# Performance work log

Measured on AMD Instinct MI355X. Metric: run time of the kernel, lower is better.

The kernel has to match this reference:

```python
import jax, jax.numpy as jnp
import numpy as np

N = 20000      # nodes
E = 320000     # edges
F = 32         # node_feat_dim
H = 128        # hidden_dim
HEADS = 4
DH = 128       # out_channels per head (PyG TransformerConv semantics)
L = 2          # number of GNNBlocks actually built


def _ln(x, s, b, eps=1e-5):
    m = x.mean(-1, keepdims=True)
    v = ((x - m) ** 2).mean(-1, keepdims=True)
    return (x - m) / jnp.sqrt(v + eps) * s + b


def setup_inputs() -> dict:
    key = jax.random.key(0)
    ks = jax.random.split(key, 16)
    nrm = lambda k, sh, sc=0.05: jax.random.normal(k, sh, dtype=jnp.float32) * sc
    inp = {}
    inp['x'] = jax.random.normal(ks[0], (N, F), dtype=jnp.float32)
    inp['edge_index'] = jax.random.randint(ks[1], (2, E), 0, N)
    inp['Win'] = nrm(ks[2], (F, H))
    inp['b_in'] = jnp.zeros((H,), jnp.float32)
    inp['ln1_s'] = jnp.ones((L, H), jnp.float32)
    inp['ln1_b'] = jnp.zeros((L, H), jnp.float32)
    inp['Wq'] = nrm(ks[3], (L, H, HEADS * DH))
    inp['bq'] = jnp.zeros((L, HEADS * DH), jnp.float32)
    inp['Wk'] = nrm(ks[4], (L, H, HEADS * DH))
    inp['bk'] = jnp.zeros((L, HEADS * DH), jnp.float32)
    inp['Wv'] = nrm(ks[5], (L, H, HEADS * DH))
    inp['bv'] = jnp.zeros((L, HEADS * DH), jnp.float32)
    inp['Wskip'] = nrm(ks[6], (L, H, H))
    inp['bskip'] = jnp.zeros((L, H), jnp.float32)
    inp['Wbeta'] = nrm(ks[7], (L, 3 * H, 1))
    inp['ln2_s'] = jnp.ones((L, H), jnp.float32)
    inp['ln2_b'] = jnp.zeros((L, H), jnp.float32)
    inp['W1'] = nrm(ks[8], (L, H, 4 * H))
    inp['b1'] = jnp.zeros((L, 4 * H), jnp.float32)
    inp['W2'] = nrm(ks[9], (L, 4 * H, H))
    inp['b2'] = jnp.zeros((L, H), jnp.float32)
    inp['g1'] = jnp.ones((L,), jnp.float32)
    inp['g2'] = jnp.ones((L,), jnp.float32)
    inp['lno_s'] = jnp.ones((H,), jnp.float32)
    inp['lno_b'] = jnp.zeros((H,), jnp.float32)
    return inp


def reference(x, edge_index, Win, b_in, ln1_s, ln1_b, Wq, bq, Wk, bk, Wv, bv,
              Wskip, bskip, Wbeta, ln2_s, ln2_b, W1, b1, W2, b2, g1, g2,
              lno_s, lno_b):
    src, dst = edge_index[0], edge_index[1]  # messages flow src -> dst
    n = x.shape[0]
    scale = 1.0 / np.sqrt(DH).astype(np.float32)
    h = x @ Win + b_in  # [N,H]
    for l in range(L):
        # --- pre-norm TransformerConv (heads=4, concat=False, beta=True) ---
        hn = _ln(h, ln1_s[l], ln1_b[l])
        q = (hn @ Wq[l] + bq[l]).reshape(n, HEADS, DH)
        k = (hn @ Wk[l] + bk[l]).reshape(n, HEADS, DH)
        v = (hn @ Wv[l] + bv[l]).reshape(n, HEADS, DH)
        # per-edge attention logits [E, HEADS]
        alpha = jnp.einsum('ehd,ehd->eh', q[dst], k[src]) * scale
        # segment softmax over incoming edges of each target node
        amax = jax.ops.segment_max(alpha, dst, num_segments=n)  # [N,HEADS]
        num = jnp.exp(alpha - amax[dst])
        den = jax.ops.segment_sum(num, dst, num_segments=n)      # [N,HEADS]
        a = num / den[dst]                                       # [E,HEADS]
        # scatter-aggregate weighted values, then mean over heads (concat=False)
        agg = jax.ops.segment_sum(a[:, :, None] * v[src], dst, num_segments=n)
        out = agg.mean(axis=1)                                   # [N,H]
        # root skip + beta gate
        xr = hn @ Wskip[l] + bskip[l]
        beta = jax.nn.sigmoid(
            jnp.concatenate([out, xr, out - xr], axis=-1) @ Wbeta[l])  # [N,1]
        attn = beta * xr + (1.0 - beta) * out
        h = h + g1[l] * attn
        # --- pre-norm FFN ---
        hn2 = _ln(h, ln2_s[l], ln2_b[l])
        ffn = jax.nn.gelu(hn2 @ W1[l] + b1[l], approximate=False) @ W2[l] + b2[l]
        h = h + g2[l] * ffn
    return _ln(h, lno_s, lno_b)
```

## Files before the change

### kernel.cpp

```cpp
#include <hip/hip_runtime.h>
#include <hip/hip_bf16.h>
#include <math.h>

#define NN 20000
#define NE 320000

typedef unsigned short ushort_t;
typedef unsigned short ushortx8 __attribute__((ext_vector_type(8)));
typedef short s16x8 __attribute__((ext_vector_type(8)));
typedef float f32x4 __attribute__((ext_vector_type(4)));
typedef float f32x2 __attribute__((ext_vector_type(2)));

__device__ __forceinline__ float us2f(unsigned short u){
  return __uint_as_float(((unsigned)u) << 16);
}
__device__ __forceinline__ unsigned short f2us(float f){
  unsigned u = __float_as_uint(f);
  unsigned r = (u + 0x7fffu + ((u >> 16) & 1u)) >> 16;
  return (unsigned short)r;
}
__device__ __forceinline__ void e4m3x8_to_f32(uint2 d, float* out){
  f32x2 a = __builtin_amdgcn_cvt_pk_f32_fp8(d.x, false);
  f32x2 b = __builtin_amdgcn_cvt_pk_f32_fp8(d.x, true);
  f32x2 c = __builtin_amdgcn_cvt_pk_f32_fp8(d.y, false);
  f32x2 e = __builtin_amdgcn_cvt_pk_f32_fp8(d.y, true);
  out[0] = a.x; out[1] = a.y; out[2] = b.x; out[3] = b.y;
  out[4] = c.x; out[5] = c.y; out[6] = e.x; out[7] = e.y;
}
__device__ __forceinline__ uint2 f32x8_to_e4m3(const float* f){
  unsigned lo = __builtin_amdgcn_cvt_pk_fp8_f32(f[0], f[1], 0u, false);
  lo = __builtin_amdgcn_cvt_pk_fp8_f32(f[2], f[3], lo, true);
  unsigned hi = __builtin_amdgcn_cvt_pk_fp8_f32(f[4], f[5], 0u, false);
  hi = __builtin_amdgcn_cvt_pk_fp8_f32(f[6], f[7], hi, true);
  return make_uint2(lo, hi);
}

__global__ void k_hist(const int* __restrict__ ei, int* __restrict__ deg){
  int e = blockIdx.x * 256 + threadIdx.x;
  if (e < NE) atomicAdd(&deg[ei[NE + e]], 1);
}

__global__ __launch_bounds__(1024) void k_scan(const int* __restrict__ deg,
                                               int* __restrict__ rowst,
                                               int* __restrict__ cur){
  __shared__ int ws[16];
  int tid = threadIdx.x;
  int lane = tid & 63, wid = tid >> 6;
  int carry = 0;
  for (int base = 0; base < NN; base += 1024){
    int i = base + tid;
    int v = (i < NN) ? deg[i] : 0;
    int incl = v;
    #pragma unroll
    for (int off = 1; off < 64; off <<= 1){
      int t = __shfl_up(incl, off);
      if (lane >= off) incl += t;
    }
    if (lane == 63) ws[wid] = incl;
    __syncthreads();
    int tot = 0, woff = 0;
    #pragma unroll
    for (int k2 = 0; k2 < 16; k2++){
      int wv = ws[k2];
      tot += wv;
      if (k2 < wid) woff += wv;
    }
    int excl = carry + woff + incl - v;
    if (i < NN){ rowst[i] = excl; cur[i] = excl; }
    carry += tot;
    __syncthreads();
  }
  if (tid == 0) rowst[NN] = carry;
}

__global__ void k_scatter(const int* __restrict__ ei, int* __restrict__ cur,
                          int* __restrict__ srcs){
  int e = blockIdx.x * 256 + threadIdx.x;
  if (e < NE){
    int s = ei[e];
    int d = ei[NE + e];
    int p = atomicAdd(&cur[d], 1);
    srcs[p] = s;
  }
}

__global__ void k_wt(const float* __restrict__ Wq, const float* __restrict__ Wk,
                     const float* __restrict__ Wv, const float* __restrict__ Wsk,
                     const float* __restrict__ W1, const float* __restrict__ W2,
                     const float* __restrict__ bq, const float* __restrict__ bk,
                     const float* __restrict__ bv, const float* __restrict__ bsk,
                     ushort_t* __restrict__ out, float* __restrict__ bcat,
                     int* __restrict__ deg){
  int f = blockIdx.x * 256 + threadIdx.x;
  if (f < 688128){
    float val;
    if (f < 425984){
      int l = f / 212992, idx = f % 212992;
      int n = idx / 128, kk = idx % 128;
      if (n < 512)       val = Wq[(size_t)l * 65536 + kk * 512 + n];
      else if (n < 1024) val = Wk[(size_t)l * 65536 + kk * 512 + (n - 512)];
      else if (n < 1536) val = Wv[(size_t)l * 65536 + kk * 512 + (n - 1024)];
      else               val = Wsk[(size_t)l * 16384 + kk * 128 + (n - 1536)];
    } else if (f < 557056){
      int idx = f - 425984;
      int l = idx / 65536, r = idx % 65536;
      int n = r / 128, kk = r % 128;
      val = W1[(size_t)l * 65536 + kk * 512 + n];
    } else {
      int idx = f - 557056;
      int l = idx / 65536, r = idx % 65536;
      int n = r / 512, kk = r % 512;
      val = W2[(size_t)l * 65536 + kk * 128 + n];
    }
    out[f] = f2us(val);
  } else if (f < 691456){
    int i = f - 688128;
    int l = i / 1664, c = i % 1664;
    float v;
    if (c < 512)       v = bq[l * 512 + c];
    else if (c < 1024) v = bk[l * 512 + c - 512];
    else if (c < 1536) v = bv[l * 512 + c - 1024];
    else               v = bsk[l * 128 + c - 1536];
    bcat[i] = v;
  } else if (f < 711456){
    deg[f - 691456] = 0;
  }
}

__global__ __launch_bounds__(128) void k_inproj(const float* __restrict__ x,
                                                const float* __restrict__ Win,
                                                const float* __restrict__ bin,
                                                float* __restrict__ h){
  __shared__ float sW[32 * 128];
  __shared__ float sx[16][32];
  int tid = threadIdx.x;
  for (int i = 0; i < 32; i++) sW[i * 128 + tid] = Win[i * 128 + tid];
  int r0 = blockIdx.x * 16;
  for (int rr = tid >> 5; rr < 16; rr += 4){
    int gr = r0 + rr;
    sx[rr][tid & 31] = (gr < NN) ? x[(size_t)gr * 32 + (tid & 31)] : 0.f;
  }
  __syncthreads();
  float bias = bin[tid];
  for (int r = 0; r < 16; r++){
    int gr = r0 + r;
    if (gr >= NN) break;
    float acc = bias;
    #pragma unroll
    for (int k2 = 0; k2 < 32; k2++) acc += sx[r][k2] * sW[k2 * 128 + tid];
    h[(size_t)gr * 128 + tid] = acc;
  }
}

template<int OUTBF16>
__global__ void k_ln(const float* __restrict__ in, const float* __restrict__ sc,
                     const float* __restrict__ bi, void* __restrict__ outp, int rows){
  int row = blockIdx.x * 4 + (threadIdx.x >> 6);
  int lane = threadIdx.x & 63;
  if (row >= rows) return;
  const float* p = in + (size_t)row * 128 + lane * 2;
  float x0 = p[0], x1 = p[1];
  float sum = x0 + x1;
  for (int m = 1; m < 64; m <<= 1) sum += __shfl_xor(sum, m);
  float mean = sum * (1.f / 128.f);
  float d0 = x0 - mean, d1 = x1 - mean;
  float vs = d0 * d0 + d1 * d1;
  for (int m = 1; m < 64; m <<= 1) vs += __shfl_xor(vs, m);
  float rstd = rsqrtf(vs * (1.f / 128.f) + 1e-5f);
  int d = lane * 2;
  float o0 = d0 * rstd * sc[d] + bi[d];
  float o1 = d1 * rstd * sc[d + 1] + bi[d + 1];
  if (OUTBF16){
    ushort_t* o = (ushort_t*)outp + (size_t)row * 128 + d;
    o[0] = f2us(o0); o[1] = f2us(o1);
  } else {
    float* o = (float*)outp + (size_t)row * 128 + d;
    o[0] = o0; o[1] = o1;
  }
}

template<int MODE>
__global__ __launch_bounds__(256) void k_mm(const ushort_t* __restrict__ A, int M, int K,
                                            const ushort_t* __restrict__ Bt,
                                            const float* __restrict__ bias,
                                            void* __restrict__ Cp, int ldc,
                                            const float* __restrict__ gptr,
                                            ushort_t* __restrict__ qout,
                                            unsigned char* __restrict__ kvout,
                                            ushort_t* __restrict__ xrout){
  __shared__ ushort_t smem[2 * 128 * 72];
  ushort_t* As = smem;
  ushort_t* Bs = smem + 128 * 72;
  int tid = threadIdx.x;
  int m0 = blockIdx.x * 128, n0 = blockIdx.y * 128;
  int lane = tid & 63, w = tid >> 6;
  int wm = (w >> 1) * 64, wn = (w & 1) * 64;
  int fr = lane & 15, fq = lane >> 4;
  f32x4 acc[4][4];
  #pragma unroll
  for (int i = 0; i < 4; i++)
    #pragma unroll
    for (int j = 0; j < 4; j++) acc[i][j] = (f32x4){0.f, 0.f, 0.f, 0.f};

  for (int k0 = 0; k0 < K; k0 += 64){
    __syncthreads();
    #pragma unroll
    for (int it = 0; it < 4; it++){
      int idx = it * 256 + tid;
      int row = idx >> 3, ks = (idx & 7) * 8;
      int gr = m0 + row; if (gr >= M) gr = M - 1;
      *(ushortx8*)&As[row * 72 + ks] = *(const ushortx8*)(A + (size_t)gr * K + k0 + ks);
      *(ushortx8*)&Bs[row * 72 + ks] = *(const ushortx8*)(Bt + (size_t)(n0 + row) * K + k0 + ks);
    }
    __syncthreads();
    #pragma unroll
    for (int ks = 0; ks < 64; ks += 32){
      s16x8 a[4], b[4];
      #pragma unroll
      for (int i = 0; i < 4; i++)
        a[i] = *(const s16x8*)&As[(wm + i * 16 + fr) * 72 + ks + fq * 8];
      #pragma unroll
      for (int j = 0; j < 4; j++)
        b[j] = *(const s16x8*)&Bs[(wn + j * 16 + fr) * 72 + ks + fq * 8];
      #pragma unroll
      for (int i = 0; i < 4; i++)
        #pragma unroll
        for (int j = 0; j < 4; j++)
          acc[i][j] = __builtin_amdgcn_mfma_f32_16x16x32_bf16(a[i], b[j], acc[i][j], 0, 0, 0);
    }
  }

  if (MODE == 2){
    float g = *gptr;
    #pragma unroll
    for (int i = 0; i < 4; i++){
      int grb = m0 + wm + i * 16 + fq * 4;
      #pragma unroll
      for (int r = 0; r < 4; r++){
        int gr = grb + r;
        if (gr >= M) continue;
        #pragma unroll
        for (int j = 0; j < 4; j++){
          int gc = n0 + wn + j * 16 + fr;
          float c = acc[i][j][r] + bias[gc];
          ((float*)Cp)[(size_t)gr * ldc + gc] += g * c;
        }
      }
    }
    return;
  }

  __syncthreads();
  ushort_t* Cs = smem;
  #pragma unroll
  for (int i = 0; i < 4; i++){
    int rowb = wm + i * 16 + fq * 4;
    #pragma unroll
    for (int j = 0; j < 4; j++){
      int col = wn + j * 16 + fr;
      float bv = bias[n0 + col];
      #pragma unroll
      for (int r = 0; r < 4; r++){
        float c = acc[i][j][r] + bv;
        if (MODE == 1) c = 0.5f * c * (1.f + erff(c * 0.70710678118654752f));
        Cs[(rowb + r) * 136 + col] = f2us(c);
      }
    }
  }
  __syncthreads();
  #pragma unroll
  for (int it = 0; it < 8; it++){
    int idx = it * 256 + tid;
    int row = idx >> 4, seg = idx & 15;
    int gr = m0 + row;
    if (gr >= M) continue;
    ushortx8 cv = *(const ushortx8*)&Cs[row * 136 + seg * 8];
    int gc = n0 + seg * 8;
    if (MODE == 1){
      *(ushortx8*)((ushort_t*)Cp + (size_t)gr * ldc + gc) = cv;
    } else {
      if (n0 < 512){
        *(ushortx8*)(qout + (size_t)gr * 512 + gc) = cv;
      } else if (n0 < 1536){
        float fv[8];
        #pragma unroll
        for (int t = 0; t < 8; t++) fv[t] = us2f(cv[t]);
        uint2 pk = f32x8_to_e4m3(fv);
        if (n0 < 1024){
          *(uint2*)(kvout + (size_t)gr * 1024 + (size_t)((gc - 512) >> 3) * 16) = pk;
        } else {
          *(uint2*)(kvout + (size_t)gr * 1024 + (size_t)((gc - 1024) >> 3) * 16 + 8) = pk;
        }
      } else {
        *(ushortx8*)(xrout + (size_t)gr * 128 + (gc - 1536)) = cv;
      }
    }
  }
}

__global__ void k_attn(const ushort_t* __restrict__ q, const unsigned char* __restrict__ kv8,
                       const int* __restrict__ rowst, const int* __restrict__ srcs,
                       const ushort_t* __restrict__ xr, const float* __restrict__ Wb,
                       const float* __restrict__ g1p, float* __restrict__ h,
                       const float* __restrict__ sc2, const float* __restrict__ bi2,
                       ushort_t* __restrict__ hn){
  int n = blockIdx.x * 4 + (threadIdx.x >> 6);
  int lane = threadIdx.x & 63;
  if (n >= NN) return;
  int s0 = rowst[n], s1 = rowst[n + 1];
  int deg = s1 - s0;
  float qf[8];
  {
    ushortx8 qv = *((const ushortx8*)(q + (size_t)n * 512) + lane);
    #pragma unroll
    for (int t = 0; t < 8; t++) qf[t] = us2f(qv[t]);
  }
  const float scale = 0.08838834764831845f;
  float l = 0.f;
  float acc[8] = {0.f, 0.f, 0.f, 0.f, 0.f, 0.f, 0.f, 0.f};
  for (int c0 = s0; c0 < s1; c0 += 64){
    int rem = s1 - c0; if (rem > 64) rem = 64;
    int se = (lane < rem) ? srcs[c0 + lane] : 0;
    int j = 0;
    for (; j + 4 <= rem; j += 4){
      int sv[4];
      #pragma unroll
      for (int u = 0; u < 4; u++) sv[u] = __shfl(se, j + u);
      uint4 kvd[4];
      #pragma unroll
      for (int u = 0; u < 4; u++)
        kvd[u] = *((const uint4*)(kv8 + (size_t)sv[u] * 1024) + lane);
      float p[4] = {0.f, 0.f, 0.f, 0.f};
      #pragma unroll
      for (int u = 0; u < 4; u++){
        float kf[8];
        e4m3x8_to_f32(make_uint2(kvd[u].x, kvd[u].y), kf);
        #pragma unroll
        for (int t = 0; t < 8; t++) p[u] += qf[t] * kf[t];
      }
      #pragma unroll
      for (int u = 0; u < 4; u++){
        p[u] += __shfl_xor(p[u], 1); p[u] += __shfl_xor(p[u], 2);
        p[u] += __shfl_xor(p[u], 4); p[u] += __shfl_xor(p[u], 8);
      }
      #pragma unroll
      for (int u = 0; u < 4; u++){
        float w = __expf(p[u] * scale);
        float vf[8];
        e4m3x8_to_f32(make_uint2(kvd[u].z, kvd[u].w), vf);
        l += w;
        #pragma unroll
        for (int t = 0; t < 8; t++) acc[t] += w * vf[t];
      }
    }
    for (; j < rem; j++){
      int sv0 = __shfl(se, j);
      uint4 kvd = *((const uint4*)(kv8 + (size_t)sv0 * 1024) + lane);
      float kf[8];
      e4m3x8_to_f32(make_uint2(kvd.x, kvd.y), kf);
      float p0 = 0.f;
      #pragma unroll
      for (int t = 0; t < 8; t++) p0 += qf[t] * kf[t];
      p0 += __shfl_xor(p0, 1); p0 += __shfl_xor(p0, 2);
      p0 += __shfl_xor(p0, 4); p0 += __shfl_xor(p0, 8);
      float w = __expf(p0 * scale);
      float vf[8];
      e4m3x8_to_f32(make_uint2(kvd.z, kvd.w), vf);
      l += w;
      #pragma unroll
      for (int t = 0; t < 8; t++) acc[t] += w * vf[t];
    }
  }
  float inv = deg ? (0.25f / l) : 0.f;
  #pragma unroll
  for (int t = 0; t < 8; t++){
    float r = acc[t] * inv;
    r += __shfl_xor(r, 16); r += __shfl_xor(r, 32);
    acc[t] = r;
  }
  if (lane < 16){
    int d = lane * 8;
    float xv[8];
    {
      ushortx8 xrv = *(const ushortx8*)(xr + (size_t)n * 128 + d);
      #pragma unroll
      for (int t = 0; t < 8; t++) xv[t] = us2f(xrv[t]);
    }
    float pp = 0.f;
    #pragma unroll
    for (int t = 0; t < 8; t++){
      float w0 = Wb[d + t], w1 = Wb[128 + d + t], w2 = Wb[256 + d + t];
      pp += acc[t] * (w0 + w2) + xv[t] * (w1 - w2);
    }
    pp += __shfl_xor(pp, 1); pp += __shfl_xor(pp, 2);
    pp += __shfl_xor(pp, 4); pp += __shfl_xor(pp, 8);
    float beta = 1.f / (1.f + __expf(-pp));
    float g = *g1p;
    float* hp = h + (size_t)n * 128 + d;
    float hv[8];
    {
      float4 h0 = *(const float4*)(hp);
      float4 h1 = *(const float4*)(hp + 4);
      hv[0]=h0.x; hv[1]=h0.y; hv[2]=h0.z; hv[3]=h0.w;
      hv[4]=h1.x; hv[5]=h1.y; hv[6]=h1.z; hv[7]=h1.w;
    }
    #pragma unroll
    for (int t = 0; t < 8; t++)
      hv[t] += g * (beta * xv[t] + (1.f - beta) * acc[t]);
    float s = 0.f;
    #pragma unroll
    for (int t = 0; t < 8; t++) s += hv[t];
    s += __shfl_xor(s, 1); s += __shfl_xor(s, 2);
    s += __shfl_xor(s, 4); s += __shfl_xor(s, 8);
    float mean = s * (1.f / 128.f);
    float vs = 0.f;
    #pragma unroll
    for (int t = 0; t < 8; t++){ float dd = hv[t] - mean; vs += dd * dd; }
    vs += __shfl_xor(vs, 1); vs += __shfl_xor(vs, 2);
    vs += __shfl_xor(vs, 4); vs += __shfl_xor(vs, 8);
    float rstd = rsqrtf(vs * (1.f / 128.f) + 1e-5f);
    *(float4*)(hp) = make_float4(hv[0], hv[1], hv[2], hv[3]);
    *(float4*)(hp + 4) = make_float4(hv[4], hv[5], hv[6], hv[7]);
    ushortx8 hno;
    #pragma unroll
    for (int t = 0; t < 8; t++)
      hno[t] = f2us((hv[t] - mean) * rstd * sc2[d + t] + bi2[d + t]);
    *(ushortx8*)(hn + (size_t)n * 128 + d) = hno;
  }
}

extern "C" void kernel_launch(void* const* d_in, const int* in_sizes, int n_in,
                              void* d_out, int out_size, void* d_ws, size_t ws_size,
                              hipStream_t stream){
  const float* x    = (const float*)d_in[0];
  const int*   ei   = (const int*)d_in[1];
  const float* Win  = (const float*)d_in[2];
  const float* bin  = (const float*)d_in[3];
  const float* ln1s = (const float*)d_in[4];
  const float* ln1b = (const float*)d_in[5];
  const float* Wq   = (const float*)d_in[6];
  const float* bq   = (const float*)d_in[7];
  const float* Wk   = (const float*)d_in[8];
  const float* bk   = (const float*)d_in[9];
  const float* Wv   = (const float*)d_in[10];
  const float* bv   = (const float*)d_in[11];
  const float* Wsk  = (const float*)d_in[12];
  const float* bsk  = (const float*)d_in[13];
  const float* Wbt  = (const float*)d_in[14];
  const float* ln2s = (const float*)d_in[15];
  const float* ln2b = (const float*)d_in[16];
  const float* W1   = (const float*)d_in[17];
  const float* b1   = (const float*)d_in[18];
  const float* W2   = (const float*)d_in[19];
  const float* b2   = (const float*)d_in[20];
  const float* g1   = (const float*)d_in[21];
  const float* g2   = (const float*)d_in[22];
  const float* lnos = (const float*)d_in[23];
  const float* lnob = (const float*)d_in[24];

  char* wsb = (char*)d_ws;
  size_t off = 0;
  float*         h    = (float*)(wsb + off);         off += (size_t)NN * 128 * 4;
  ushort_t*      hn   = (ushort_t*)(wsb + off);      off += (size_t)NN * 128 * 2;
  ushort_t*      qbuf = (ushort_t*)(wsb + off);      off += (size_t)NN * 512 * 2;
  unsigned char* kv8  = (unsigned char*)(wsb + off); off += (size_t)NN * 1024;
  ushort_t*      xrb  = (ushort_t*)(wsb + off);      off += (size_t)NN * 128 * 2;
  ushort_t*      tb   = (ushort_t*)(wsb + off);      off += (size_t)NN * 512 * 2;
  ushort_t*      wt   = (ushort_t*)(wsb + off);      off += (size_t)688128 * 2;
  float*         bcat = (float*)(wsb + off);         off += (size_t)3328 * 4;
  int*           deg   = (int*)(wsb + off);          off += (size_t)NN * 4;
  int*           rowst = (int*)(wsb + off);          off += (size_t)(NN + 4) * 4;
  int*           cur   = (int*)(wsb + off);          off += (size_t)NN * 4;
  int*           srcs  = (int*)(wsb + off);          off += (size_t)NE * 4;
  ushort_t* Wcat = wt;
  ushort_t* W1t  = wt + 425984;
  ushort_t* W2t  = wt + 557056;

  k_wt<<<2780, 256, 0, stream>>>(Wq, Wk, Wv, Wsk, W1, W2, bq, bk, bv, bsk, wt, bcat, deg);
  k_hist<<<(NE + 255) / 256, 256, 0, stream>>>(ei, deg);
  k_scan<<<1, 1024, 0, stream>>>(deg, rowst, cur);
  k_scatter<<<(NE + 255) / 256, 256, 0, stream>>>(ei, cur, srcs);
  k_inproj<<<(NN + 15) / 16, 128, 0, stream>>>(x, Win, bin, h);

  dim3 gQ(157, 13), gF1(157, 4), gF2(157, 1);
  for (int l = 0; l < 2; l++){
    k_ln<1><<<(NN + 3) / 4, 256, 0, stream>>>(h, ln1s + l * 128, ln1b + l * 128, hn, NN);
    k_mm<3><<<gQ, 256, 0, stream>>>(hn, NN, 128, Wcat + (size_t)l * 212992, bcat + l * 1664,
                                    nullptr, 0, nullptr, qbuf, kv8, xrb);
    k_attn<<<(NN + 3) / 4, 256, 0, stream>>>(qbuf, kv8, rowst, srcs, xrb, Wbt + l * 384,
                                             g1 + l, h, ln2s + l * 128, ln2b + l * 128, hn);
    k_mm<1><<<gF1, 256, 0, stream>>>(hn, NN, 128, W1t + (size_t)l * 65536, b1 + l * 512,
                                     tb, 512, nullptr, nullptr, nullptr, nullptr);
    k_mm<2><<<gF2, 256, 0, stream>>>(tb, NN, 512, W2t + (size_t)l * 65536, b2 + l * 128,
                                     h, 128, g2 + l, nullptr, nullptr, nullptr);
  }
  k_ln<0><<<(NN + 3) / 4, 256, 0, stream>>>(h, lnos, lnob, (float*)d_out, NN);
}
```

Measured before the change: 443.3 us.

## Remap GEMM workgroups per XCD and deepen attention gather unroll

The GEMM kernels now launch a 1D grid and remap block IDs so that consecutive tiles land on the same XCD. The aim is to share the A tile across N-blocks in each XCD's L2. The attention kernel adds an 8-wide unrolled gather loop so more independent KV loads are in flight, and it uses readlane instead of shfl to broadcast source indices. The wider unroll raises register pressure and could lower occupancy.

```diff
diff --git a/kernel.cpp b/kernel.cpp
--- a/kernel.cpp
+++ b/kernel.cpp
@@ -187,12 +187,19 @@
                                             const float* __restrict__ gptr,
                                             ushort_t* __restrict__ qout,
                                             unsigned char* __restrict__ kvout,
-                                            ushort_t* __restrict__ xrout){
+                                            ushort_t* __restrict__ xrout,
+                                            int nbn){
   __shared__ ushort_t smem[2 * 128 * 72];
   ushort_t* As = smem;
   ushort_t* Bs = smem + 128 * 72;
   int tid = threadIdx.x;
-  int m0 = blockIdx.x * 128, n0 = blockIdx.y * 128;
+  int nwg = gridDim.x;
+  int orig = blockIdx.x;
+  int q8 = nwg >> 3, r8 = nwg & 7;
+  int xcd = orig & 7, jj = orig >> 3;
+  int wgid = (xcd < r8) ? (xcd * (q8 + 1) + jj)
+                        : (r8 * (q8 + 1) + (xcd - r8) * q8 + jj);
+  int m0 = (wgid / nbn) * 128, n0 = (wgid % nbn) * 128;
   int lane = tid & 63, w = tid >> 6;
   int wm = (w >> 1) * 64, wn = (w & 1) * 64;
   int fr = lane & 15, fq = lane >> 4;
@@ -316,36 +323,54 @@
     for (int t = 0; t < 8; t++) qf[t] = us2f(qv[t]);
   }
   const float scale = 0.08838834764831845f;
+  const uint4* kvb = (const uint4*)kv8;
   float l = 0.f;
   float acc[8] = {0.f, 0.f, 0.f, 0.f, 0.f, 0.f, 0.f, 0.f};
   for (int c0 = s0; c0 < s1; c0 += 64){
     int rem = s1 - c0; if (rem > 64) rem = 64;
     int se = (lane < rem) ? srcs[c0 + lane] : 0;
     int j = 0;
+    for (; j + 8 <= rem; j += 8){
+      uint4 kvd[8];
+      #pragma unroll
+      for (int u = 0; u < 8; u++){
+        int sv = __builtin_amdgcn_readlane(se, j + u);
+        kvd[u] = kvb[(size_t)sv * 64 + lane];
+      }
+      #pragma unroll
+      for (int u = 0; u < 8; u++){
+        float kf[8];
+        e4m3x8_to_f32(make_uint2(kvd[u].x, kvd[u].y), kf);
+        float p = 0.f;
+        #pragma unroll
+        for (int t = 0; t < 8; t++) p += qf[t] * kf[t];
+        p += __shfl_xor(p, 1); p += __shfl_xor(p, 2);
+        p += __shfl_xor(p, 4); p += __shfl_xor(p, 8);
+        float w = __expf(p * scale);
+        float vf[8];
+        e4m3x8_to_f32(make_uint2(kvd[u].z, kvd[u].w), vf);
+        l += w;
+        #pragma unroll
+        for (int t = 0; t < 8; t++) acc[t] += w * vf[t];
+      }
+    }
     for (; j + 4 <= rem; j += 4){
-      int sv[4];
-      #pragma unroll
-      for (int u = 0; u < 4; u++) sv[u] = __shfl(se, j + u);
       uint4 kvd[4];
       #pragma unroll
-      for (int u = 0; u < 4; u++)
-        kvd[u] = *((const uint4*)(kv8 + (size_t)sv[u] * 1024) + lane);
-      float p[4] = {0.f, 0.f, 0.f, 0.f};
+      for (int u = 0; u < 4; u++){
+        int sv = __builtin_amdgcn_readlane(se, j + u);
+        kvd[u] = kvb[(size_t)sv * 64 + lane];
+      }
       #pragma unroll
       for (int u = 0; u < 4; u++){
         float kf[8];
         e4m3x8_to_f32(make_uint2(kvd[u].x, kvd[u].y), kf);
-        #pragma unroll
-        for (int t = 0; t < 8; t++) p[u] += qf[t] * kf[t];
-      }
-      #pragma unroll
-      for (int u = 0; u < 4; u++){
-        p[u] += __shfl_xor(p[u], 1); p[u] += __shfl_xor(p[u], 2);
-        p[u] += __shfl_xor(p[u], 4); p[u] += __shfl_xor(p[u], 8);
-      }
-      #pragma unroll
-      for (int u = 0; u < 4; u++){
-        float w = __expf(p[u] * scale);
+        float p = 0.f;
+        #pragma unroll
+        for (int t = 0; t < 8; t++) p += qf[t] * kf[t];
+        p += __shfl_xor(p, 1); p += __shfl_xor(p, 2);
+        p += __shfl_xor(p, 4); p += __shfl_xor(p, 8);
+        float w = __expf(p * scale);
         float vf[8];
         e4m3x8_to_f32(make_uint2(kvd[u].z, kvd[u].w), vf);
         l += w;
@@ -354,8 +379,8 @@
       }
     }
     for (; j < rem; j++){
-      int sv0 = __shfl(se, j);
-      uint4 kvd = *((const uint4*)(kv8 + (size_t)sv0 * 1024) + lane);
+      int sv0 = __builtin_amdgcn_readlane(se, j);
+      uint4 kvd = kvb[(size_t)sv0 * 64 + lane];
       float kf[8];
       e4m3x8_to_f32(make_uint2(kvd.x, kvd.y), kf);
       float p0 = 0.f;
@@ -482,17 +507,16 @@
   k_scatter<<<(NE + 255) / 256, 256, 0, stream>>>(ei, cur, srcs);
   k_inproj<<<(NN + 15) / 16, 128, 0, stream>>>(x, Win, bin, h);
 
-  dim3 gQ(157, 13), gF1(157, 4), gF2(157, 1);
   for (int l = 0; l < 2; l++){
     k_ln<1><<<(NN + 3) / 4, 256, 0, stream>>>(h, ln1s + l * 128, ln1b + l * 128, hn, NN);
-    k_mm<3><<<gQ, 256, 0, stream>>>(hn, NN, 128, Wcat + (size_t)l * 212992, bcat + l * 1664,
-                                    nullptr, 0, nullptr, qbuf, kv8, xrb);
+    k_mm<3><<<157 * 13, 256, 0, stream>>>(hn, NN, 128, Wcat + (size_t)l * 212992, bcat + l * 1664,
+                                          nullptr, 0, nullptr, qbuf, kv8, xrb, 13);
     k_attn<<<(NN + 3) / 4, 256, 0, stream>>>(qbuf, kv8, rowst, srcs, xrb, Wbt + l * 384,
                                              g1 + l, h, ln2s + l * 128, ln2b + l * 128, hn);
-    k_mm<1><<<gF1, 256, 0, stream>>>(hn, NN, 128, W1t + (size_t)l * 65536, b1 + l * 512,
-                                     tb, 512, nullptr, nullptr, nullptr, nullptr);
-    k_mm<2><<<gF2, 256, 0, stream>>>(tb, NN, 512, W2t + (size_t)l * 65536, b2 + l * 128,
-                                     h, 128, g2 + l, nullptr, nullptr, nullptr);
+    k_mm<1><<<157 * 4, 256, 0, stream>>>(hn, NN, 128, W1t + (size_t)l * 65536, b1 + l * 512,
+                                         tb, 512, nullptr, nullptr, nullptr, nullptr, 4);
+    k_mm<2><<<157, 256, 0, stream>>>(tb, NN, 512, W2t + (size_t)l * 65536, b2 + l * 128,
+                                     h, 128, g2 + l, nullptr, nullptr, nullptr, 1);
   }
   k_ln<0><<<(NN + 3) / 4, 256, 0, stream>>>(h, lnos, lnob, (float*)d_out, NN);
 }
```

Result: faster. 434.4 us (-2.0%).
